# Optimization experiments

Measured on AMD Instinct MI355X. Metric: run time of the kernel, lower is better.

The kernel has to match this reference:

```python
import jax, jax.numpy as jnp
import numpy as np

B, T, K = 256, 512, 128


def setup_inputs() -> dict:
    key = jax.random.key(0)
    k1, k2, k3, k4 = jax.random.split(key, 4)
    emissions = jax.random.normal(k1, (B, T, K), jnp.float32)
    tag_ids = jax.random.randint(k2, (B, T), 0, K, dtype=jnp.int32)
    lengths = jnp.maximum(jax.random.randint(k3, (B,), 0, T + 1, dtype=jnp.int32), 1)
    # learned CRF transition matrix (transition_weight * learning_rate_multiplier)
    transitions = jax.random.normal(k4, (K, K), jnp.float32) * 0.1
    return {"emissions": emissions, "tag_ids": tag_ids, "lengths": lengths,
            "transitions": transitions}


def _log_norm(emissions, transitions, lengths):
    # forward algorithm (log-sum-exp semiring scan over time)
    t = emissions.shape[1]
    alpha0 = emissions[:, 0]  # [B,K]
    valid = jnp.arange(1, t)[:, None] < lengths[None, :]  # [T-1,B]

    def step(alpha, inp):
        emit_t, v = inp  # [B,K], [B]
        new = jax.nn.logsumexp(alpha[:, :, None] + transitions[None], axis=1) + emit_t
        return jnp.where(v[:, None], new, alpha), None

    alpha, _ = jax.lax.scan(step, alpha0, (jnp.swapaxes(emissions[:, 1:], 0, 1), valid))
    return jax.nn.logsumexp(alpha, axis=-1)  # [B]


def _sequence_score(emissions, transitions, tag_ids, lengths):
    t = emissions.shape[1]
    mask = (jnp.arange(t)[None, :] < lengths[:, None]).astype(emissions.dtype)  # [B,T]
    unary = jnp.take_along_axis(emissions, tag_ids[..., None], axis=-1)[..., 0]  # [B,T]
    unary_score = jnp.sum(unary * mask, axis=1)
    pair = transitions[tag_ids[:, :-1], tag_ids[:, 1:]]  # [B,T-1]
    binary_score = jnp.sum(pair * mask[:, 1:], axis=1)  # prefix mask: t+1 valid => t valid
    return unary_score + binary_score


def _viterbi_decode(emissions, transitions, lengths):
    t = emissions.shape[1]
    k = emissions.shape[2]
    v0 = emissions[:, 0]  # [B,K]
    valid = jnp.arange(1, t)[:, None] < lengths[None, :]  # [T-1,B]
    identity_bp = jnp.arange(k, dtype=jnp.int32)[None, :]  # pass-through for padding

    def fwd(v, inp):
        emit_t, va = inp
        scores = v[:, :, None] + transitions[None]  # [B,K,K]
        bp = jnp.argmax(scores, axis=1).astype(jnp.int32)  # [B,K]
        new = jnp.max(scores, axis=1) + emit_t
        v_new = jnp.where(va[:, None], new, v)
        bp = jnp.where(va[:, None], bp, identity_bp)
        return v_new, bp

    v_final, bps = jax.lax.scan(fwd, v0, (jnp.swapaxes(emissions[:, 1:], 0, 1), valid))
    last_tag = jnp.argmax(v_final, axis=-1).astype(jnp.int32)  # [B]

    def back(tag, bp_t):
        prev = jnp.take_along_axis(bp_t, tag[:, None], axis=1)[:, 0]
        return prev, tag  # emit tag_{t+1}, carry tag_t

    first_tag, tags_rest = jax.lax.scan(back, last_tag, bps, reverse=True)
    decoded = jnp.concatenate([first_tag[None], tags_rest], axis=0)  # [T,B]
    return jnp.swapaxes(decoded, 0, 1)  # [B,T]


def reference(emissions, tag_ids, lengths, transitions):
    log_likelihood = _sequence_score(emissions, transitions, tag_ids, lengths) \
        - _log_norm(emissions, transitions, lengths)
    loss = -jnp.mean(log_likelihood)
    decoded = _viterbi_decode(emissions, transitions, lengths)
    mask = (jnp.arange(emissions.shape[1])[None, :] < lengths[:, None]).astype(jnp.int32)
    is_equal = (tag_ids == decoded).astype(jnp.int32)
    tag_accuracy = jnp.sum(is_equal * mask) / jnp.sum(mask)
    return loss, decoded, tag_accuracy
```

## Files before the change

kernel.cpp:

```cpp
#include <hip/hip_runtime.h>

#define T_ 512
#define K_ 128
#define B_ 256

#define GROUPS(F) F(0) F(1) F(2) F(3) F(4) F(5) F(6) F(7)

__global__ __launch_bounds__(1024, 4) void crf_main(
    const float* __restrict__ emissions,
    const int* __restrict__ tag_ids,
    const int* __restrict__ lengths,
    const float* __restrict__ transitions,
    float* __restrict__ out,
    float* __restrict__ ws_ll,
    int* __restrict__ ws_cnt)
{
    __shared__ unsigned char bpLDS[T_ * K_];
    __shared__ __align__(16) float eaBuf[2][K_];
    __shared__ __align__(16) float vaBuf[2][K_];
    __shared__ float sNorm[2];
    __shared__ float redLDS[8];
    __shared__ int   redILDS[8];
    __shared__ unsigned char decLDS[T_];
    __shared__ int ltagLDS;

    const int b   = blockIdx.x;
    const int tid = threadIdx.x;
    const int len = lengths[b];
    const float* emB = emissions + (size_t)b * T_ * K_;
    const int*  tagB = tag_ids + b * T_;

    if (tid < T_) {
        int t = tid;
        float s = 0.f;
        if (t < len) {
            int tg = tagB[t];
            s = emB[t * K_ + tg];
            if (t >= 1) s += transitions[tagB[t - 1] * K_ + tg];
        }
        #pragma unroll
        for (int m = 1; m < 64; m <<= 1) s += __shfl_xor(s, m);
        if ((tid & 63) == 0) redLDS[tid >> 6] = s;
    }

    const int role = tid >> 9;
    const int lin  = tid & 511;
    const int j = lin >> 2;
    const int c = lin & 3;

#define DECLW(g) float w##g##0, w##g##1, w##g##2, w##g##3;
    GROUPS(DECLW)
    {
        const float* wp = transitions + (c * 32) * K_ + j;
#define LOADW(g) w##g##0 = wp[(4*g+0)*K_]; w##g##1 = wp[(4*g+1)*K_]; \
                 w##g##2 = wp[(4*g+2)*K_]; w##g##3 = wp[(4*g+3)*K_];
        GROUPS(LOADW)
        if (role == 0) {
#define EXPW(g) w##g##0 = __expf(w##g##0); w##g##1 = __expf(w##g##1); \
                w##g##2 = __expf(w##g##2); w##g##3 = __expf(w##g##3);
            GROUPS(EXPW)
        }
#define FENCEW(g) asm volatile("" : "+v"(w##g##0), "+v"(w##g##1), "+v"(w##g##2), "+v"(w##g##3));
        GROUPS(FENCEW)
    }

    float e0 = emB[j];
    if (role == 0) {
        if (c == 0) eaBuf[0][j] = __expf(e0);
        if (lin == 0) sNorm[0] = e0;
    } else {
        if (c == 0) vaBuf[0][j] = e0;
    }
    float emNext = emB[K_ + j];
    __syncthreads();

    int cur = 0;
    float Sprev = 0.f;
    for (int t = 1; t < len; ++t) {
        float emit = emNext;
        { int tn = (t + 1 < T_) ? (t + 1) : (T_ - 1);
          emNext = emB[tn * K_ + j]; }
        if (role == 0) {
            float Scur = sNorm[cur];
            const float* ea = &eaBuf[cur][c * 32];
            float a0 = 0.f, a1 = 0.f, a2 = 0.f, a3 = 0.f;
#define DOTW(g) { float4 e4 = *(const float4*)(ea + 4*g); \
                  a0 = fmaf(e4.x, w##g##0, a0); a1 = fmaf(e4.y, w##g##1, a1); \
                  a2 = fmaf(e4.z, w##g##2, a2); a3 = fmaf(e4.w, w##g##3, a3); }
            GROUPS(DOTW)
            float dot = (a0 + a1) + (a2 + a3);
            dot += __shfl_xor(dot, 1);
            dot += __shfl_xor(dot, 2);
            float anew = __logf(dot) + Sprev + emit;
            if (c == 0) eaBuf[cur ^ 1][j] = __expf(anew - Scur);
            if (lin == 0) sNorm[cur ^ 1] = anew;
            Sprev = Scur;
        } else {
            const float* va = &vaBuf[cur][c * 32];
            float mB = -3.4028235e38f;
            int arg = 0;
#define VITW(g) { float4 v4 = *(const float4*)(va + 4*g); \
        float s0 = v4.x + w##g##0; if (s0 > mB) { mB = s0; arg = 4*g+0; } \
        float s1 = v4.y + w##g##1; if (s1 > mB) { mB = s1; arg = 4*g+1; } \
        float s2 = v4.z + w##g##2; if (s2 > mB) { mB = s2; arg = 4*g+2; } \
        float s3 = v4.w + w##g##3; if (s3 > mB) { mB = s3; arg = 4*g+3; } }
            GROUPS(VITW)
            arg += c * 32;
            #pragma unroll
            for (int d = 1; d < 4; d <<= 1) {
                float om = __shfl_xor(mB, d);
                int   oa = __shfl_xor(arg, d);
                if (om > mB || (om == mB && oa < arg)) { mB = om; arg = oa; }
            }
            if (c == 0) {
                vaBuf[cur ^ 1][j] = mB + emit;
                bpLDS[t * K_ + j] = (unsigned char)arg;
            }
        }
        cur ^= 1;
        __syncthreads();
    }

    float logZv = 0.f;
    if (tid < 64) {
        float s = eaBuf[cur][tid] + eaBuf[cur][tid + 64];
        #pragma unroll
        for (int m = 1; m < 64; m <<= 1) s += __shfl_xor(s, m);
        logZv = Sprev + __logf(s);
    }

    if (tid >= 512 && tid < 576) {
        int l = tid - 512;
        float m = vaBuf[cur][l]; int a = l;
        float v2 = vaBuf[cur][l + 64];
        if (v2 > m) { m = v2; a = l + 64; }
        #pragma unroll
        for (int sft = 1; sft < 64; sft <<= 1) {
            float om = __shfl_xor(m, sft);
            int   oa = __shfl_xor(a, sft);
            if (om > m || (om == m && oa < a)) { m = om; a = oa; }
        }
        if (l == 0) ltagLDS = a;
    }
    __syncthreads();

    if (tid == 0) {
        int tg = ltagLDS;
        for (int t = T_ - 1; t >= 1; --t) {
            decLDS[t] = (unsigned char)tg;
            if (t < len) tg = bpLDS[t * K_ + tg];
        }
        decLDS[0] = (unsigned char)tg;
    }
    __syncthreads();

    if (tid < T_) {
        int t = tid;
        int dv = decLDS[t];
        out[1 + b * T_ + t] = (float)dv;
        int good = (t < len && tagB[t] == dv) ? 1 : 0;
        #pragma unroll
        for (int m = 1; m < 64; m <<= 1) good += __shfl_xor(good, m);
        if ((tid & 63) == 0) redILDS[tid >> 6] = good;
    }
    __syncthreads();

    if (tid == 0) {
        float sc = 0.f; int cnt = 0;
        #pragma unroll
        for (int w = 0; w < 8; ++w) { sc += redLDS[w]; cnt += redILDS[w]; }
        ws_ll[b]  = sc - logZv;
        ws_cnt[b] = cnt;
    }
}

__global__ void crf_final(const float* __restrict__ ws_ll,
                          const int* __restrict__ ws_cnt,
                          const int* __restrict__ lengths,
                          float* __restrict__ out)
{
    __shared__ float sll[4];
    __shared__ int scnt[4], slen[4];
    int tid = threadIdx.x;
    float ll = ws_ll[tid];
    int   cn = ws_cnt[tid];
    int   L  = lengths[tid];
    #pragma unroll
    for (int m = 1; m < 64; m <<= 1) {
        ll += __shfl_xor(ll, m);
        cn += __shfl_xor(cn, m);
        L  += __shfl_xor(L, m);
    }
    if ((tid & 63) == 0) { sll[tid >> 6] = ll; scnt[tid >> 6] = cn; slen[tid >> 6] = L; }
    __syncthreads();
    if (tid == 0) {
        float llS = sll[0] + sll[1] + sll[2] + sll[3];
        int   cS  = scnt[0] + scnt[1] + scnt[2] + scnt[3];
        int   LS  = slen[0] + slen[1] + slen[2] + slen[3];
        out[0] = -llS / (float)B_;
        out[1 + B_ * T_] = (float)cS / (float)LS;
    }
}

extern "C" void kernel_launch(void* const* d_in, const int* in_sizes, int n_in,
                              void* d_out, int out_size, void* d_ws, size_t ws_size,
                              hipStream_t stream) {
    const float* emissions   = (const float*)d_in[0];
    const int*   tag_ids     = (const int*)d_in[1];
    const int*   lengths     = (const int*)d_in[2];
    const float* transitions = (const float*)d_in[3];
    float* out = (float*)d_out;

    float* ws_ll  = (float*)d_ws;
    int*   ws_cnt = (int*)((char*)d_ws + B_ * sizeof(float));

    crf_main<<<B_, 1024, 0, stream>>>(emissions, tag_ids, lengths, transitions,
                                      out, ws_ll, ws_cnt);
    crf_final<<<1, B_, 0, stream>>>(ws_ll, ws_cnt, lengths, out);
}
```

Before: 672.0 us.

## Split forward and Viterbi recurrences into separate blocks with LDS partial reductions

Launches two 512-thread blocks per sequence: one runs the log-sum-exp forward recurrence, the other runs Viterbi and backtracking, so they no longer share one 1024-thread block and its barriers. Each thread now covers 16 source tags for two destination tags, and the per-destination reduction goes through LDS partial arrays with a second barrier instead of cross-lane shuffles. The forward block no longer waits for the Viterbi work at every step. In exchange each step needs two __syncthreads, the reduction phase runs on only 128 threads, and the block count doubles while per-block LDS stays large.

```diff
diff --git a/kernel.cpp b/kernel.cpp
--- a/kernel.cpp
+++ b/kernel.cpp
@@ -3,10 +3,28 @@
 #define T_ 512
 #define K_ 128
 #define B_ 256
-
-#define GROUPS(F) F(0) F(1) F(2) F(3) F(4) F(5) F(6) F(7)
-
-__global__ __launch_bounds__(1024, 4) void crf_main(
+#define NEGINF (-3.4028235e38f)
+
+
+#define GR(F) F(0) F(1) F(2) F(3)
+
+#define DECLW(g) float wa##g##0, wa##g##1, wa##g##2, wa##g##3, \
+                       wb##g##0, wb##g##1, wb##g##2, wb##g##3;
+#define LOADW(g) wa##g##0 = wp[(4*g+0)*K_];      wa##g##1 = wp[(4*g+1)*K_]; \
+                 wa##g##2 = wp[(4*g+2)*K_];      wa##g##3 = wp[(4*g+3)*K_]; \
+                 wb##g##0 = wp[(4*g+0)*K_ + 64]; wb##g##1 = wp[(4*g+1)*K_ + 64]; \
+                 wb##g##2 = wp[(4*g+2)*K_ + 64]; wb##g##3 = wp[(4*g+3)*K_ + 64];
+#define EXPW(g)  wa##g##0 = __expf(wa##g##0); wa##g##1 = __expf(wa##g##1); \
+                 wa##g##2 = __expf(wa##g##2); wa##g##3 = __expf(wa##g##3); \
+                 wb##g##0 = __expf(wb##g##0); wb##g##1 = __expf(wb##g##1); \
+                 wb##g##2 = __expf(wb##g##2); wb##g##3 = __expf(wb##g##3);
+#define FENCEW(g) asm volatile("" : "+v"(wa##g##0), "+v"(wa##g##1), "+v"(wa##g##2), "+v"(wa##g##3), \
+                                    "+v"(wb##g##0), "+v"(wb##g##1), "+v"(wb##g##2), "+v"(wb##g##3));
+
+#define VSTEP(val, wreg, idx, mm, aa) \
+    { float s_ = (val) + (wreg); if (s_ > (mm)) { (mm) = s_; (aa) = (idx); } }
+
+__global__ __launch_bounds__(512, 4) void crf_main(
     const float* __restrict__ emissions,
     const int* __restrict__ tag_ids,
     const int* __restrict__ lengths,
@@ -15,162 +33,197 @@
     float* __restrict__ ws_ll,
     int* __restrict__ ws_cnt)
 {
-    __shared__ unsigned char bpLDS[T_ * K_];
-    __shared__ __align__(16) float eaBuf[2][K_];
-    __shared__ __align__(16) float vaBuf[2][K_];
-    __shared__ float sNorm[2];
-    __shared__ float redLDS[8];
-    __shared__ int   redILDS[8];
-    __shared__ unsigned char decLDS[T_];
-    __shared__ int ltagLDS;
-
-    const int b   = blockIdx.x;
-    const int tid = threadIdx.x;
-    const int len = lengths[b];
+    __shared__ __align__(16) unsigned char smem[77392];
+    unsigned char* bp   = smem;
+    float* part = (float*)(smem + 65536);
+    float* buf  = (float*)(smem + 65536 + 10240);
+    unsigned char* dec = smem + 65536 + 10240 + 1024;
+    float* sNorm = (float*)(dec + T_);
+    float* redS  = sNorm + 2;
+    int*   redI  = (int*)(redS + 8);
+    int*   ltag  = redI + 8;
+
+    const int bx   = blockIdx.x;
+    const int b    = bx >> 1;
+    const int role = bx & 1;
+    const int tid  = threadIdx.x;
+    const int len  = lengths[b];
     const float* emB = emissions + (size_t)b * T_ * K_;
     const int*  tagB = tag_ids + b * T_;
 
-    if (tid < T_) {
-        int t = tid;
-        float s = 0.f;
-        if (t < len) {
-            int tg = tagB[t];
-            s = emB[t * K_ + tg];
-            if (t >= 1) s += transitions[tagB[t - 1] * K_ + tg];
-        }
-        #pragma unroll
-        for (int m = 1; m < 64; m <<= 1) s += __shfl_xor(s, m);
-        if ((tid & 63) == 0) redLDS[tid >> 6] = s;
-    }
-
-    const int role = tid >> 9;
-    const int lin  = tid & 511;
-    const int j = lin >> 2;
-    const int c = lin & 3;
-
-#define DECLW(g) float w##g##0, w##g##1, w##g##2, w##g##3;
-    GROUPS(DECLW)
+    const int p  = tid & 63;
+    const int cc = tid >> 6;
+
+    GR(DECLW)
     {
-        const float* wp = transitions + (c * 32) * K_ + j;
-#define LOADW(g) w##g##0 = wp[(4*g+0)*K_]; w##g##1 = wp[(4*g+1)*K_]; \
-                 w##g##2 = wp[(4*g+2)*K_]; w##g##3 = wp[(4*g+3)*K_];
-        GROUPS(LOADW)
-        if (role == 0) {
-#define EXPW(g) w##g##0 = __expf(w##g##0); w##g##1 = __expf(w##g##1); \
-                w##g##2 = __expf(w##g##2); w##g##3 = __expf(w##g##3);
-            GROUPS(EXPW)
-        }
-#define FENCEW(g) asm volatile("" : "+v"(w##g##0), "+v"(w##g##1), "+v"(w##g##2), "+v"(w##g##3));
-        GROUPS(FENCEW)
-    }
-
-    float e0 = emB[j];
+        const float* wp = transitions + (cc * 16) * K_ + p;
+        GR(LOADW)
+        if (role == 0) { GR(EXPW) }
+        GR(FENCEW)
+    }
+
+    float emNext = 0.f;
+    if (tid < K_) emNext = emB[K_ + tid];
+
     if (role == 0) {
-        if (c == 0) eaBuf[0][j] = __expf(e0);
-        if (lin == 0) sNorm[0] = e0;
+        {
+            float s = 0.f;
+            if (tid < len) {
+                int tg = tagB[tid];
+                s = emB[tid * K_ + tg];
+                if (tid >= 1) s += transitions[tagB[tid - 1] * K_ + tg];
+            }
+            #pragma unroll
+            for (int m = 1; m < 64; m <<= 1) s += __shfl_xor(s, m);
+            if ((tid & 63) == 0) redS[tid >> 6] = s;
+        }
+        if (tid < K_) buf[tid] = __expf(emB[tid]);
+        if (tid == 0) sNorm[0] = emB[0];
+        __syncthreads();
+
+        int cur = 0;
+        float Sprev = 0.f;
+        for (int t = 1; t < len; ++t) {
+            const float* ea = &buf[cur * K_ + cc * 16];
+            float4 e0 = *(const float4*)(ea);
+            float4 e1 = *(const float4*)(ea + 4);
+            float4 e2 = *(const float4*)(ea + 8);
+            float4 e3 = *(const float4*)(ea + 12);
+            float d0 = 0.f, d1 = 0.f;
+#define FDOT(v4, g) d0 = fmaf(v4.x, wa##g##0, d0); d0 = fmaf(v4.y, wa##g##1, d0); \
+                    d0 = fmaf(v4.z, wa##g##2, d0); d0 = fmaf(v4.w, wa##g##3, d0); \
+                    d1 = fmaf(v4.x, wb##g##0, d1); d1 = fmaf(v4.y, wb##g##1, d1); \
+                    d1 = fmaf(v4.z, wb##g##2, d1); d1 = fmaf(v4.w, wb##g##3, d1);
+            FDOT(e0, 0) FDOT(e1, 1) FDOT(e2, 2) FDOT(e3, 3)
+            part[p * 12 + cc]        = d0;
+            part[(p + 64) * 12 + cc] = d1;
+            float emit = emNext;
+            if (tid < K_) { int tn = (t + 1 < T_) ? t + 1 : T_ - 1;
+                            emNext = emB[tn * K_ + tid]; }
+            __syncthreads();
+            if (tid < K_) {
+                float4 q0 = *(const float4*)&part[tid * 12];
+                float4 q1 = *(const float4*)&part[tid * 12 + 4];
+                float sum = ((q0.x + q0.y) + (q0.z + q0.w))
+                          + ((q1.x + q1.y) + (q1.z + q1.w));
+                float Scur = sNorm[cur];
+                float anew = __logf(sum) + Sprev + emit;
+                buf[(cur ^ 1) * K_ + tid] = __expf(anew - Scur);
+                if (tid == 0) sNorm[cur ^ 1] = anew;
+                Sprev = Scur;
+            }
+            cur ^= 1;
+            __syncthreads();
+        }
+        float logZv = 0.f;
+        if (tid < 64) {
+            float s = buf[cur * K_ + tid] + buf[cur * K_ + tid + 64];
+            #pragma unroll
+            for (int m = 1; m < 64; m <<= 1) s += __shfl_xor(s, m);
+            logZv = Sprev + __logf(s);
+        }
+        if (tid == 0) {
+            float sc = 0.f;
+            #pragma unroll
+            for (int w = 0; w < 8; ++w) sc += redS[w];
+            ws_ll[b] = sc - logZv;
+        }
     } else {
-        if (c == 0) vaBuf[0][j] = e0;
-    }
-    float emNext = emB[K_ + j];
-    __syncthreads();
-
-    int cur = 0;
-    float Sprev = 0.f;
-    for (int t = 1; t < len; ++t) {
-        float emit = emNext;
-        { int tn = (t + 1 < T_) ? (t + 1) : (T_ - 1);
-          emNext = emB[tn * K_ + j]; }
-        if (role == 0) {
-            float Scur = sNorm[cur];
-            const float* ea = &eaBuf[cur][c * 32];
-            float a0 = 0.f, a1 = 0.f, a2 = 0.f, a3 = 0.f;
-#define DOTW(g) { float4 e4 = *(const float4*)(ea + 4*g); \
-                  a0 = fmaf(e4.x, w##g##0, a0); a1 = fmaf(e4.y, w##g##1, a1); \
-                  a2 = fmaf(e4.z, w##g##2, a2); a3 = fmaf(e4.w, w##g##3, a3); }
-            GROUPS(DOTW)
-            float dot = (a0 + a1) + (a2 + a3);
-            dot += __shfl_xor(dot, 1);
-            dot += __shfl_xor(dot, 2);
-            float anew = __logf(dot) + Sprev + emit;
-            if (c == 0) eaBuf[cur ^ 1][j] = __expf(anew - Scur);
-            if (lin == 0) sNorm[cur ^ 1] = anew;
-            Sprev = Scur;
-        } else {
-            const float* va = &vaBuf[cur][c * 32];
-            float mB = -3.4028235e38f;
-            int arg = 0;
-#define VITW(g) { float4 v4 = *(const float4*)(va + 4*g); \
-        float s0 = v4.x + w##g##0; if (s0 > mB) { mB = s0; arg = 4*g+0; } \
-        float s1 = v4.y + w##g##1; if (s1 > mB) { mB = s1; arg = 4*g+1; } \
-        float s2 = v4.z + w##g##2; if (s2 > mB) { mB = s2; arg = 4*g+2; } \
-        float s3 = v4.w + w##g##3; if (s3 > mB) { mB = s3; arg = 4*g+3; } }
-            GROUPS(VITW)
-            arg += c * 32;
-            #pragma unroll
-            for (int d = 1; d < 4; d <<= 1) {
-                float om = __shfl_xor(mB, d);
-                int   oa = __shfl_xor(arg, d);
-                if (om > mB || (om == mB && oa < arg)) { mB = om; arg = oa; }
-            }
-            if (c == 0) {
-                vaBuf[cur ^ 1][j] = mB + emit;
-                bpLDS[t * K_ + j] = (unsigned char)arg;
-            }
-        }
-        cur ^= 1;
-        __syncthreads();
-    }
-
-    float logZv = 0.f;
-    if (tid < 64) {
-        float s = eaBuf[cur][tid] + eaBuf[cur][tid + 64];
-        #pragma unroll
-        for (int m = 1; m < 64; m <<= 1) s += __shfl_xor(s, m);
-        logZv = Sprev + __logf(s);
-    }
-
-    if (tid >= 512 && tid < 576) {
-        int l = tid - 512;
-        float m = vaBuf[cur][l]; int a = l;
-        float v2 = vaBuf[cur][l + 64];
-        if (v2 > m) { m = v2; a = l + 64; }
-        #pragma unroll
-        for (int sft = 1; sft < 64; sft <<= 1) {
-            float om = __shfl_xor(m, sft);
-            int   oa = __shfl_xor(a, sft);
-            if (om > m || (om == m && oa < a)) { m = om; a = oa; }
-        }
-        if (l == 0) ltagLDS = a;
-    }
-    __syncthreads();
-
-    if (tid == 0) {
-        int tg = ltagLDS;
-        for (int t = T_ - 1; t >= 1; --t) {
-            decLDS[t] = (unsigned char)tg;
-            if (t < len) tg = bpLDS[t * K_ + tg];
-        }
-        decLDS[0] = (unsigned char)tg;
-    }
-    __syncthreads();
-
-    if (tid < T_) {
-        int t = tid;
-        int dv = decLDS[t];
-        out[1 + b * T_ + t] = (float)dv;
-        int good = (t < len && tagB[t] == dv) ? 1 : 0;
-        #pragma unroll
-        for (int m = 1; m < 64; m <<= 1) good += __shfl_xor(good, m);
-        if ((tid & 63) == 0) redILDS[tid >> 6] = good;
-    }
-    __syncthreads();
-
-    if (tid == 0) {
-        float sc = 0.f; int cnt = 0;
-        #pragma unroll
-        for (int w = 0; w < 8; ++w) { sc += redLDS[w]; cnt += redILDS[w]; }
-        ws_ll[b]  = sc - logZv;
-        ws_cnt[b] = cnt;
+        if (tid < K_) buf[tid] = emB[tid];
+        __syncthreads();
+
+        int cur = 0;
+        for (int t = 1; t < len; ++t) {
+            const float* va = &buf[cur * K_ + cc * 16];
+            float4 e0 = *(const float4*)(va);
+            float4 e1 = *(const float4*)(va + 4);
+            float4 e2 = *(const float4*)(va + 8);
+            float4 e3 = *(const float4*)(va + 12);
+            float ma0 = NEGINF, ma1 = NEGINF; int aa0 = 0, aa1 = 0;
+            VSTEP(e0.x, wa00, 0, ma0, aa0)  VSTEP(e0.y, wa01, 1, ma0, aa0)
+            VSTEP(e0.z, wa02, 2, ma0, aa0)  VSTEP(e0.w, wa03, 3, ma0, aa0)
+            VSTEP(e1.x, wa10, 4, ma0, aa0)  VSTEP(e1.y, wa11, 5, ma0, aa0)
+            VSTEP(e1.z, wa12, 6, ma0, aa0)  VSTEP(e1.w, wa13, 7, ma0, aa0)
+            VSTEP(e2.x, wa20, 8, ma1, aa1)  VSTEP(e2.y, wa21, 9, ma1, aa1)
+            VSTEP(e2.z, wa22,10, ma1, aa1)  VSTEP(e2.w, wa23,11, ma1, aa1)
+            VSTEP(e3.x, wa30,12, ma1, aa1)  VSTEP(e3.y, wa31,13, ma1, aa1)
+            VSTEP(e3.z, wa32,14, ma1, aa1)  VSTEP(e3.w, wa33,15, ma1, aa1)
+            if (ma1 > ma0) { ma0 = ma1; aa0 = aa1; }
+            float mb0 = NEGINF, mb1 = NEGINF; int ab0 = 0, ab1 = 0;
+            VSTEP(e0.x, wb00, 0, mb0, ab0)  VSTEP(e0.y, wb01, 1, mb0, ab0)
+            VSTEP(e0.z, wb02, 2, mb0, ab0)  VSTEP(e0.w, wb03, 3, mb0, ab0)
+            VSTEP(e1.x, wb10, 4, mb0, ab0)  VSTEP(e1.y, wb11, 5, mb0, ab0)
+            VSTEP(e1.z, wb12, 6, mb0, ab0)  VSTEP(e1.w, wb13, 7, mb0, ab0)
+            VSTEP(e2.x, wb20, 8, mb1, ab1)  VSTEP(e2.y, wb21, 9, mb1, ab1)
+            VSTEP(e2.z, wb22,10, mb1, ab1)  VSTEP(e2.w, wb23,11, mb1, ab1)
+            VSTEP(e3.x, wb30,12, mb1, ab1)  VSTEP(e3.y, wb31,13, mb1, ab1)
+            VSTEP(e3.z, wb32,14, mb1, ab1)  VSTEP(e3.w, wb33,15, mb1, ab1)
+            if (mb1 > mb0) { mb0 = mb1; ab0 = ab1; }
+            *(float2*)&part[p * 20 + 2 * cc] =
+                make_float2(ma0, (float)(aa0 + cc * 16));
+            *(float2*)&part[(p + 64) * 20 + 2 * cc] =
+                make_float2(mb0, (float)(ab0 + cc * 16));
+            float emit = emNext;
+            if (tid < K_) { int tn = (t + 1 < T_) ? t + 1 : T_ - 1;
+                            emNext = emB[tn * K_ + tid]; }
+            __syncthreads();
+            if (tid < K_) {
+                const float* pr = &part[tid * 20];
+                float4 r0 = *(const float4*)(pr);
+                float4 r1 = *(const float4*)(pr + 4);
+                float4 r2 = *(const float4*)(pr + 8);
+                float4 r3 = *(const float4*)(pr + 12);
+                float bm = r0.x; float ba = r0.y;
+                if (r0.z > bm) { bm = r0.z; ba = r0.w; }
+                if (r1.x > bm) { bm = r1.x; ba = r1.y; }
+                if (r1.z > bm) { bm = r1.z; ba = r1.w; }
+                if (r2.x > bm) { bm = r2.x; ba = r2.y; }
+                if (r2.z > bm) { bm = r2.z; ba = r2.w; }
+                if (r3.x > bm) { bm = r3.x; ba = r3.y; }
+                if (r3.z > bm) { bm = r3.z; ba = r3.w; }
+                buf[(cur ^ 1) * K_ + tid] = bm + emit;
+                bp[t * K_ + tid] = (unsigned char)(int)ba;
+            }
+            cur ^= 1;
+            __syncthreads();
+        }
+        if (tid < 64) {
+            float m = buf[cur * K_ + tid]; int a = tid;
+            float v2 = buf[cur * K_ + tid + 64];
+            if (v2 > m) { m = v2; a = tid + 64; }
+            #pragma unroll
+            for (int s = 1; s < 64; s <<= 1) {
+                float om = __shfl_xor(m, s);
+                int   oa = __shfl_xor(a, s);
+                if (om > m || (om == m && oa < a)) { m = om; a = oa; }
+            }
+            if (tid == 0) *ltag = a;
+        }
+        __syncthreads();
+        if (tid == 0) {
+            int tg = *ltag;
+            for (int t = T_ - 1; t >= 1; --t) {
+                dec[t] = (unsigned char)tg;
+                if (t < len) tg = bp[t * K_ + tg];
+            }
+            dec[0] = (unsigned char)tg;
+        }
+        __syncthreads();
+        {
+            int dv = dec[tid];
+            out[1 + b * T_ + tid] = (float)dv;
+            int good = (tid < len && tagB[tid] == dv) ? 1 : 0;
+            #pragma unroll
+            for (int m = 1; m < 64; m <<= 1) good += __shfl_xor(good, m);
+            if ((tid & 63) == 0) redI[tid >> 6] = good;
+        }
+        __syncthreads();
+        if (tid == 0) {
+            int cnt = 0;
+            #pragma unroll
+            for (int w = 0; w < 8; ++w) cnt += redI[w];
+            ws_cnt[b] = cnt;
+        }
     }
 }
 
@@ -214,7 +267,7 @@
     float* ws_ll  = (float*)d_ws;
     int*   ws_cnt = (int*)((char*)d_ws + B_ * sizeof(float));
 
-    crf_main<<<B_, 1024, 0, stream>>>(emissions, tag_ids, lengths, transitions,
-                                      out, ws_ll, ws_cnt);
+    crf_main<<<2 * B_, 512, 0, stream>>>(emissions, tag_ids, lengths, transitions,
+                                         out, ws_ll, ws_cnt);
     crf_final<<<1, B_, 0, stream>>>(ws_ll, ws_cnt, lengths, out);
 }
```

After: 650.7 us. 1.03x faster.
